# Kernel tuning notes

Hardware: AMD Instinct MI355X
Metric: run time of the kernel (lower is better)

Reference implementation:

```python
import jax, jax.numpy as jnp
import numpy as np

C, H, K, G = 256, 8, 32, 8
HD = C // H
SCALE = HD ** -0.5
POS_BND = int(0.8 * K * 1 ** 0.5)  # 25
RPE_NUM = 2 * POS_BND + 1          # 51
NW = 4096


def setup_inputs() -> dict:
    key = jax.random.key(0)
    ks = jax.random.split(key, 8)
    data = jax.random.normal(ks[0], (NW * (K + G), C), dtype=jnp.float32)
    # relative xyz offsets between points in a window; exercise the clamp
    rel_pos = jax.random.randint(ks[1], (NW, K, K, 3), -POS_BND - 5, POS_BND + 6).astype(jnp.int32)
    # additive mask: 0 for valid pairs, -100 for masked (padded) pairs
    keep = jax.random.bernoulli(ks[2], 0.9, (NW, K + G, K + G))
    mask = jnp.where(keep, 0.0, -100.0).astype(jnp.float32)
    qkv_w = jax.random.normal(ks[3], (C, 3 * C), dtype=jnp.float32) * (C ** -0.5)
    qkv_b = jnp.zeros((3 * C,), dtype=jnp.float32)
    proj_w = jax.random.normal(ks[4], (C, C), dtype=jnp.float32) * (C ** -0.5)
    proj_b = jnp.zeros((C,), dtype=jnp.float32)
    rpe_table = jax.random.normal(ks[5], (3 * RPE_NUM, H), dtype=jnp.float32) * 0.02
    return {"data": data, "rel_pos": rel_pos, "mask": mask, "qkv_w": qkv_w,
            "qkv_b": qkv_b, "proj_w": proj_w, "proj_b": proj_b, "rpe_table": rpe_table}


def reference(data, rel_pos, mask, qkv_w, qkv_b, proj_w, proj_b, rpe_table):
    W = K + G  # window size including context tokens
    qkv = data @ qkv_w + qkv_b                              # (T, 3C)
    qkv_std = jnp.std(qkv, axis=0, ddof=1)                  # torch .std is unbiased
    qkv = qkv.reshape(-1, W, 3, H, HD).transpose(2, 0, 3, 1, 4)  # (3, Nw, H, W, HD)
    q, k, v = qkv[0] * SCALE, qkv[1], qkv[2]
    attn = jnp.einsum('nhqd,nhkd->nhqk', q, k)              # (Nw, H, W, W)
    # RPE: clamp offsets, index per-axis slices of table, sum over xyz
    idx = jnp.clip(rel_pos, -POS_BND, POS_BND) + POS_BND + jnp.arange(3, dtype=rel_pos.dtype) * RPE_NUM
    rpe = rpe_table[idx].sum(axis=3)                        # (Nw, K, K, H)
    rpe = rpe.transpose(0, 3, 1, 2)                         # (Nw, H, K, K)
    rpe = jnp.pad(rpe, ((0, 0), (0, 0), (G, 0), (G, 0)))    # pad for context tokens
    attn = attn + rpe + mask[:, None]
    attn = jax.nn.softmax(attn, axis=-1)
    out = jnp.einsum('nhqk,nhkd->nqhd', attn, v).reshape(-1, W, C)
    out = out @ proj_w + proj_b                             # (Nw, W, C)
    return (out, qkv_std)
```

## Files before the change

### kernel.cpp

```cpp
#include <hip/hip_runtime.h>
#include <math.h>

#define SCALE_F 0.17677669529663687f

typedef __bf16 bf16x8 __attribute__((ext_vector_type(8)));
typedef float f32x4 __attribute__((ext_vector_type(4)));

__device__ __forceinline__ unsigned short f2bf(float f) {
  unsigned u = __builtin_bit_cast(unsigned, f);
  u = (u + 0x7FFFu + ((u >> 16) & 1u)) >> 16;
  return (unsigned short)u;
}
__device__ __forceinline__ float bf2f(unsigned short u) {
  return __builtin_bit_cast(float, (unsigned)u << 16);
}
__device__ __forceinline__ unsigned pk2(float a, float b) {
  return (unsigned)f2bf(a) | ((unsigned)f2bf(b) << 16);
}
__device__ __forceinline__ bf16x8 ld16(const void* p) {
  int4 v = *(const int4*)p;
  return __builtin_bit_cast(bf16x8, v);
}
__device__ __forceinline__ void gll16(const void* g, void* l) {
  __builtin_amdgcn_global_load_lds(
      (const __attribute__((address_space(1))) unsigned int*)g,
      (__attribute__((address_space(3))) unsigned int*)l, 16, 0, 0);
}


__global__ void octa_prep2(const float* __restrict__ qkv_w, const float* __restrict__ proj_w,
                           unsigned short* __restrict__ wTq, unsigned short* __restrict__ pTq)
{
  int e = blockIdx.x * 256 + threadIdx.x;
  if (e < 196608) {
    int nh = e / 98304, rr = e % 98304;
    int kc = rr / 12288, p2 = rr % 12288;
    int n = p2 >> 5, cw = p2 & 31;
    int kl = cw ^ (((n >> 1) & 3) << 3);
    wTq[e] = f2bf(qkv_w[(size_t)(kc * 32 + kl) * 768 + nh * 384 + n]);
  } else {
    int e2 = e - 196608;
    int kc = e2 >> 13, p2 = e2 & 8191;
    int n = p2 >> 5, cw = p2 & 31;
    int kl = cw ^ (((n >> 1) & 3) << 3);
    pTq[e2] = f2bf(proj_w[(size_t)(kc * 32 + kl) * 256 + n]);
  }
}

#define KQ_A  0
#define KQ_B0 32768
#define KQ_B1 57344
#define KQ_E  32768
#define KQ_LDS 81920

__global__ __launch_bounds__(512, 4)
void octa_qkv(const float* __restrict__ data, const float* __restrict__ qkv_b,
              const unsigned short* __restrict__ wTq, float* __restrict__ ws,
              char* __restrict__ qg, char* __restrict__ kg, char* __restrict__ vg)
{
  extern __shared__ char smem[];
  const int tid = threadIdx.x, lane = tid & 63, wid = tid >> 6;
  const int ql = lane & 15, lg = lane >> 4;
  const int bm = blockIdx.x >> 1, nh = blockIdx.x & 1;
  const int wr = wid >> 2, wc = wid & 3;
  const char* wbase = (const char*)wTq + (size_t)nh * 196608;

  #pragma unroll
  for (int it = 0; it < 3; ++it)
    gll16(wbase + wid * 3072 + it * 1024 + lane * 16,
          smem + KQ_B0 + wid * 3072 + it * 1024);
  {
    const float4* src = (const float4*)(data + (size_t)bm * 64 * 256);
    #pragma unroll
    for (int rep = 0; rep < 8; ++rep) {
      int f = rep * 512 + tid;
      int row = f >> 6, q4 = f & 63;
      float4 d4 = src[f];
      *(uint2*)(smem + KQ_A + row * 512 + ((q4 * 8) ^ ((row & 7) << 4))) =
          make_uint2(pk2(d4.x, d4.y), pk2(d4.z, d4.w));
    }
  }
  __syncthreads();

  f32x4 acc[2][6];
  #pragma unroll
  for (int m = 0; m < 2; ++m)
    #pragma unroll
    for (int n = 0; n < 6; ++n) acc[m][n] = (f32x4){0.f, 0.f, 0.f, 0.f};

  #pragma unroll
  for (int t = 0; t < 8; ++t) {
    if (t < 7) {
      char* bb1 = smem + (((t + 1) & 1) ? KQ_B1 : KQ_B0);
      #pragma unroll
      for (int it = 0; it < 3; ++it)
        gll16(wbase + (size_t)(t + 1) * 24576 + wid * 3072 + it * 1024 + lane * 16,
              bb1 + wid * 3072 + it * 1024);
    }
    const char* bb = smem + ((t & 1) ? KQ_B1 : KQ_B0);
    bf16x8 af[2];
    #pragma unroll
    for (int mt = 0; mt < 2; ++mt) {
      int row = wr * 32 + mt * 16 + ql;
      af[mt] = ld16(smem + KQ_A + row * 512 + ((t * 64 + lg * 16) ^ ((row & 7) << 4)));
    }
    #pragma unroll
    for (int nt = 0; nt < 6; ++nt) {
      int n = wc * 96 + nt * 16 + ql;
      bf16x8 bf = ld16(bb + n * 64 + ((lg * 16) ^ (((n >> 1) & 3) << 4)));
      acc[0][nt] = __builtin_amdgcn_mfma_f32_16x16x32_bf16(af[0], bf, acc[0][nt], 0, 0, 0);
      acc[1][nt] = __builtin_amdgcn_mfma_f32_16x16x32_bf16(af[1], bf, acc[1][nt], 0, 0, 0);
    }
    __syncthreads();
  }

  #pragma unroll
  for (int nt = 0; nt < 6; ++nt) {
    int col_l = wc * 96 + nt * 16 + ql;
    int gcol = nh * 384 + col_l;
    int tensor = gcol >> 8;
    float bias = qkv_b[gcol];
    float s1 = 0.f, s2 = 0.f;
    #pragma unroll
    for (int mt = 0; mt < 2; ++mt)
      #pragma unroll
      for (int r = 0; r < 4; ++r) {
        int tok = wr * 32 + mt * 16 + lg * 4 + r;
        float v = acc[mt][nt][r] + bias;
        s1 += v; s2 += v * v;
        float sv = (tensor == 0) ? v * SCALE_F : v;
        *(unsigned short*)(smem + KQ_E + tok * 768 + ((col_l * 2) ^ ((tok & 7) << 4))) = f2bf(sv);
      }
    s1 += __shfl_xor(s1, 16); s1 += __shfl_xor(s1, 32);
    s2 += __shfl_xor(s2, 16); s2 += __shfl_xor(s2, 32);
    if (lg == 0) { atomicAdd(ws + gcol, s1); atomicAdd(ws + 768 + gcol, s2); }
  }
  __syncthreads();

  #pragma unroll
  for (int rep = 0; rep < 6; ++rep) {
    int c = rep * 512 + tid;
    int tok_l = c / 48, cc = c - tok_l * 48;
    int4 val = *(const int4*)(smem + KQ_E + tok_l * 768 + ((cc * 16) ^ ((tok_l & 7) << 4)));
    int gcol0 = nh * 384 + cc * 8;
    int tensor = gcol0 >> 8, h = (gcol0 >> 5) & 7, d0 = gcol0 & 31;
    int tg = bm * 64 + tok_l, w = tg / 40, tk = tg - w * 40;
    size_t slice = (size_t)(w * 8 + h) * 2560;
    char* base = tensor == 0 ? qg : (tensor == 1 ? kg : vg);
    *(int4*)(base + slice + tk * 64 + d0 * 2) = val;
  }
}

#define A2_MSK 0
#define A2_IDX 4160
#define A2_RPT 8256
#define A2_P   13376
#define A2_LDS 44096

__global__ __launch_bounds__(512, 4)
void octa_attn(const char* __restrict__ qg, const char* __restrict__ kg,
               const char* __restrict__ vg, const float* __restrict__ maskp,
               const int* __restrict__ rel_pos, const float* __restrict__ rpe_table,
               char* __restrict__ Og)
{
  extern __shared__ char smem[];
  const int tid = threadIdx.x, w = blockIdx.x, wid = tid >> 6;
  const int lane = tid & 63, ql = lane & 15, lg = lane >> 4, h = wid;
  const int perm = ql * 64 + lg * 16;
  const char* qb = qg + (size_t)(w * 8 + h) * 2560;
  const char* kb = kg + (size_t)(w * 8 + h) * 2560;
  const char* vb = vg + (size_t)(w * 8 + h) * 2560;

  bf16x8 kf0 = ld16(kb + perm), kf1 = ld16(kb + 1024 + perm), kf2 = ld16(kb + 2048 + perm);
  bf16x8 qf0 = ld16(qb + perm), qf1 = ld16(qb + 1024 + perm), qf2 = ld16(qb + 2048 + perm);
  union U8 { unsigned short u[8]; bf16x8 v; };
  U8 ua, ub, uc, ud;
  #pragma unroll
  for (int j = 0; j < 8; ++j) {
    int tok = lg * 8 + j;
    ua.u[j] = *(const unsigned short*)(vb + tok * 64 + ql * 2);
    ub.u[j] = *(const unsigned short*)(vb + tok * 64 + (16 + ql) * 2);
  }
  if (lg == 0) {
    #pragma unroll
    for (int j = 0; j < 8; ++j) {
      uc.u[j] = *(const unsigned short*)(vb + (32 + j) * 64 + ql * 2);
      ud.u[j] = *(const unsigned short*)(vb + (32 + j) * 64 + (16 + ql) * 2);
    }
  } else {
    #pragma unroll
    for (int j = 0; j < 8; ++j) { uc.u[j] = 0; ud.u[j] = 0; }
  }
  bf16x8 vA = ua.v, vB = ub.v, vC = uc.v, vD = ud.v;

  for (int f = tid; f < 1600; f += 512) {
    float m = maskp[(size_t)w * 1600 + f];
    int qi = f / 40, kj = f - qi * 40;
    *(unsigned short*)(smem + A2_MSK + kj * 104 + qi * 2) = f2bf(m);
  }
  for (int f = tid; f < 1024; f += 512) {
    const int* rp = rel_pos + ((size_t)w * 1024 + f) * 3;
    int c0 = rp[0], c1 = rp[1], c2 = rp[2];
    c0 = min(25, max(-25, c0)); c1 = min(25, max(-25, c1)); c2 = min(25, max(-25, c2));
    unsigned pk = (unsigned)(c0 + 25) | ((unsigned)(c1 + 76) << 10) | ((unsigned)(c2 + 127) << 20);
    int qi8 = f >> 5, kj8 = f & 31;
    *(unsigned*)(smem + A2_IDX + kj8 * 128 + ((qi8 * 4) ^ ((kj8 & 1) << 6))) = pk;
  }
  for (int f = tid; f < 1224; f += 512)
    *(float*)(smem + A2_RPT + (((f & 7) * 160 + (f >> 3)) << 2)) = rpe_table[f];
  __syncthreads();

  f32x4 st[9];
  {
    bf16x8 kf[3] = {kf0, kf1, kf2}, qf[3] = {qf0, qf1, qf2};
    #pragma unroll
    for (int a = 0; a < 3; ++a)
      #pragma unroll
      for (int b = 0; b < 3; ++b)
        st[a * 3 + b] = __builtin_amdgcn_mfma_f32_16x16x32_bf16(
            kf[a], qf[b], (f32x4){0.f, 0.f, 0.f, 0.f}, 0, 0, 0);
  }

  float mx[3] = {-3e38f, -3e38f, -3e38f};
  #pragma unroll
  for (int a = 0; a < 3; ++a) {
    #pragma unroll
    for (int b = 0; b < 3; ++b) {
      #pragma unroll
      for (int r = 0; r < 4; ++r) {
        int kj = a * 16 + lg * 4 + r;
        int qi = b * 16 + ql;
        float s = st[a * 3 + b][r];
        if (kj < 40) {
          if (qi < 40) {
            s += bf2f(*(const unsigned short*)(smem + A2_MSK + kj * 104 + qi * 2));
            if (kj >= 8 && qi >= 8) {
              unsigned pk = *(const unsigned*)(smem + A2_IDX + (kj - 8) * 128 +
                                               (((qi - 8) * 4) ^ (((kj - 8) & 1) << 6)));
              s += *(const float*)(smem + A2_RPT + ((h * 160 + (pk & 1023)) << 2))
                 + *(const float*)(smem + A2_RPT + ((h * 160 + ((pk >> 10) & 1023)) << 2))
                 + *(const float*)(smem + A2_RPT + ((h * 160 + (pk >> 20)) << 2));
            }
          }
        } else {
          s = -1e30f;
        }
        st[a * 3 + b][r] = s;
        mx[b] = fmaxf(mx[b], s);
      }
    }
  }
  #pragma unroll
  for (int b = 0; b < 3; ++b) {
    mx[b] = fmaxf(mx[b], __shfl_xor(mx[b], 16));
    mx[b] = fmaxf(mx[b], __shfl_xor(mx[b], 32));
  }
  float sum[3] = {0.f, 0.f, 0.f};
  #pragma unroll
  for (int a = 0; a < 3; ++a)
    #pragma unroll
    for (int b = 0; b < 3; ++b)
      #pragma unroll
      for (int r = 0; r < 4; ++r) {
        float e = __expf(st[a * 3 + b][r] - mx[b]);
        st[a * 3 + b][r] = e;
        sum[b] += e;
      }
  float inv[3];
  #pragma unroll
  for (int b = 0; b < 3; ++b) {
    sum[b] += __shfl_xor(sum[b], 16);
    sum[b] += __shfl_xor(sum[b], 32);
    inv[b] = 1.f / sum[b];
  }

  char* pb_ = smem + A2_P + wid * 3840;
  f32x4 ot[6];
  #pragma unroll
  for (int i = 0; i < 6; ++i) ot[i] = (f32x4){0.f, 0.f, 0.f, 0.f};

  #pragma unroll
  for (int a = 0; a < 2; ++a)
    #pragma unroll
    for (int b = 0; b < 3; ++b)
      #pragma unroll
      for (int r = 0; r < 4; ++r) {
        int kj = a * 16 + lg * 4 + r, qi = b * 16 + ql;
        *(unsigned short*)(pb_ + qi * 80 + kj * 2) = f2bf(st[a * 3 + b][r] * inv[b]);
      }
  asm volatile("" ::: "memory");
  #pragma unroll
  for (int b = 0; b < 3; ++b) {
    bf16x8 pf = ld16(pb_ + (b * 16 + ql) * 80 + lg * 16);
    ot[b]     = __builtin_amdgcn_mfma_f32_16x16x32_bf16(vA, pf, ot[b], 0, 0, 0);
    ot[3 + b] = __builtin_amdgcn_mfma_f32_16x16x32_bf16(vB, pf, ot[3 + b], 0, 0, 0);
  }
  asm volatile("" ::: "memory");
  #pragma unroll
  for (int b = 0; b < 3; ++b) {
    int qi = b * 16 + ql;
    #pragma unroll
    for (int r = 0; r < 4; ++r)
      *(unsigned short*)(pb_ + qi * 80 + (lg * 4 + r) * 2) = f2bf(st[6 + b][r] * inv[b]);
    *(uint2*)(pb_ + qi * 80 + 32 + lg * 8) = make_uint2(0u, 0u);
  }
  asm volatile("" ::: "memory");
  #pragma unroll
  for (int b = 0; b < 3; ++b) {
    bf16x8 pf = ld16(pb_ + (b * 16 + ql) * 80 + lg * 16);
    ot[b]     = __builtin_amdgcn_mfma_f32_16x16x32_bf16(vC, pf, ot[b], 0, 0, 0);
    ot[3 + b] = __builtin_amdgcn_mfma_f32_16x16x32_bf16(vD, pf, ot[3 + b], 0, 0, 0);
  }

  __syncthreads();
  #pragma unroll
  for (int dm = 0; dm < 2; ++dm)
    #pragma unroll
    for (int b = 0; b < 3; ++b) {
      int qi = b * 16 + ql;
      if (b == 2 && ql >= 8) continue;
      unsigned u0 = pk2(ot[dm * 3 + b][0], ot[dm * 3 + b][1]);
      unsigned u1 = pk2(ot[dm * 3 + b][2], ot[dm * 3 + b][3]);
      int tg = w * 40 + qi;
      int colb = (h * 32 + dm * 16 + lg * 4) * 2;
      *(uint2*)(Og + (size_t)tg * 512 + (colb ^ (((tg >> 1) & 3) << 4))) = make_uint2(u0, u1);
    }
}

#define P3_A0 0
#define P3_A1 8192
#define P3_B0 16384
#define P3_B1 32768
#define P3_LDS 49152

__global__ __launch_bounds__(512, 4)
void octa_proj(const char* __restrict__ Og, const unsigned short* __restrict__ pTq,
               const float* __restrict__ proj_b, float* __restrict__ out)
{
  extern __shared__ char smem[];
  const int tid = threadIdx.x, lane = tid & 63, wid = tid >> 6;
  const int ql = lane & 15, lg = lane >> 4;
  const int bm = blockIdx.x;
  const int wr = wid >> 2, wc = wid & 3;
  const char* pbase = (const char*)pTq;

  gll16(Og + ((size_t)bm * 128 + (tid >> 2)) * 512 + (tid & 3) * 16,
        smem + P3_A0 + wid * 1024);
  #pragma unroll
  for (int it = 0; it < 2; ++it)
    gll16(pbase + (wid * 128 + it * 64 + lane) * 16, smem + P3_B0 + wid * 2048 + it * 1024);
  __syncthreads();

  f32x4 acc[4][4];
  #pragma unroll
  for (int m = 0; m < 4; ++m)
    #pragma unroll
    for (int n = 0; n < 4; ++n) acc[m][n] = (f32x4){0.f, 0.f, 0.f, 0.f};

  #pragma unroll
  for (int t = 0; t < 8; ++t) {
    if (t < 7) {
      char* ab1 = smem + (((t + 1) & 1) ? P3_A1 : P3_A0);
      char* bb1 = smem + (((t + 1) & 1) ? P3_B1 : P3_B0);
      gll16(Og + ((size_t)bm * 128 + (tid >> 2)) * 512 + (t + 1) * 64 + (tid & 3) * 16,
            ab1 + wid * 1024);
      #pragma unroll
      for (int it = 0; it < 2; ++it)
        gll16(pbase + (size_t)(t + 1) * 16384 + (wid * 128 + it * 64 + lane) * 16,
              bb1 + wid * 2048 + it * 1024);
    }
    const char* ab = smem + ((t & 1) ? P3_A1 : P3_A0);
    const char* bb = smem + ((t & 1) ? P3_B1 : P3_B0);
    bf16x8 af[4];
    #pragma unroll
    for (int mt = 0; mt < 4; ++mt) {
      int row = wr * 64 + mt * 16 + ql;
      af[mt] = ld16(ab + row * 64 + ((lg * 16) ^ (((row >> 1) & 3) << 4)));
    }
    #pragma unroll
    for (int nt = 0; nt < 4; ++nt) {
      int n = wc * 64 + nt * 16 + ql;
      bf16x8 bf = ld16(bb + n * 64 + ((lg * 16) ^ (((n >> 1) & 3) << 4)));
      #pragma unroll
      for (int mt = 0; mt < 4; ++mt)
        acc[mt][nt] = __builtin_amdgcn_mfma_f32_16x16x32_bf16(af[mt], bf, acc[mt][nt], 0, 0, 0);
    }
    __syncthreads();
  }

  #pragma unroll
  for (int nt = 0; nt < 4; ++nt) {
    int col = wc * 64 + nt * 16 + ql;
    float pb = proj_b[col];
    #pragma unroll
    for (int mt = 0; mt < 4; ++mt)
      #pragma unroll
      for (int r = 0; r < 4; ++r) {
        int tg = bm * 128 + wr * 64 + mt * 16 + lg * 4 + r;
        out[(size_t)tg * 256 + col] = acc[mt][nt][r] + pb;
      }
  }
}

__global__ void octa_std(const float* __restrict__ ws, float* __restrict__ out,
                         int total_rows, size_t off)
{
  int j = blockIdx.x * 256 + threadIdx.x;
  if (j < 768) {
    float s = ws[j], ss = ws[768 + j];
    float T = (float)total_rows;
    float var = (ss - s * s / T) / (T - 1.f);
    out[off + j] = sqrtf(fmaxf(var, 0.f));
  }
}

#define O_RPE 0
#define O_MSK 4896
#define O_IDX 8096
#define O_A   12192
#define O_ATT 36768
#define B1_SZ 49152
#define ATT_STRIDE 11776
#define AK 3840
#define AV 7680
#define B2_S (O_ATT + 94208)
#define B2_A O_ATT
#define LDS_BYTES_V4 163744

__device__ __forceinline__ int a_addr(int row, int byte) {
  return O_A + row * 512 + (byte ^ ((row & 7) << 4));
}
__device__ __forceinline__ int v_addr(int d, int byte) {
  return AV + d * 128 + (byte ^ ((d & 7) << 4));
}

__global__ void octa_prep_v4(const float* __restrict__ qkv_w, const float* __restrict__ proj_w,
                             unsigned short* __restrict__ wTq, unsigned short* __restrict__ pTq)
{
  int idx = blockIdx.x * 256 + threadIdx.x;
  if (idx < 196608) {
    int n = idx >> 8, k = idx & 255;
    wTq[idx] = f2bf(qkv_w[k * 768 + n]);
  } else {
    int i = idx - 196608;
    int n = i >> 8, k = i & 255;
    pTq[i] = f2bf(proj_w[k * 256 + n]);
  }
}

__global__ __launch_bounds__(512, 2)
void octa_main_v4(const float* __restrict__ data, const int* __restrict__ rel_pos,
                  const float* __restrict__ maskp, const float* __restrict__ qkv_b,
                  const float* __restrict__ proj_b, const float* __restrict__ rpe_table,
                  const unsigned short* __restrict__ wTq, const unsigned short* __restrict__ pTq,
                  float* __restrict__ ws, float* __restrict__ out)
{
  extern __shared__ char smem[];
  float* s_rpe = (float*)(smem + O_RPE);
  const int tid = threadIdx.x;
  const int w   = blockIdx.x;
  const int wid = tid >> 6;
  const int lane = tid & 63;
  const int ql = lane & 15;
  const int lg = lane >> 4;
  const int h  = wid;
  const int ab = O_ATT + wid * ATT_STRIDE;

  {
    #pragma unroll
    for (int it = 0; it < 6; ++it) {
      int g = it * 512 + tid;
      int n = g >> 2, slot = g & 3;
      const char* src = (const char*)wTq + (size_t)n * 512 + ((slot * 16) ^ ((n & 3) << 4));
      gll16(src, smem + O_ATT + it * 8192 + wid * 1024);
    }
  }
  for (int f = tid; f < 1224; f += 512) s_rpe[f] = rpe_table[f];
  for (int f = tid; f < 400; f += 512) {
    float4 m4 = ((const float4*)(maskp + (size_t)w * 1600))[f];
    uint2 pk;
    pk.x = pk2(m4.x, m4.y); pk.y = pk2(m4.z, m4.w);
    *(uint2*)(smem + O_MSK + f * 8) = pk;
  }
  for (int p = tid; p < 1024; p += 512) {
    const int* rp = rel_pos + ((size_t)w * 1024 + p) * 3;
    int c0 = rp[0], c1 = rp[1], c2 = rp[2];
    c0 = min(25, max(-25, c0)); c1 = min(25, max(-25, c1)); c2 = min(25, max(-25, c2));
    unsigned pk = (unsigned)(c0 + 25) | ((unsigned)(c1 + 76) << 10) | ((unsigned)(c2 + 127) << 20);
    *(unsigned*)(smem + O_IDX + ((p * 4) ^ (((p >> 5) & 7) << 4))) = pk;
  }
  {
    const float4* src = (const float4*)(data + (size_t)w * 10240);
    for (int f = tid; f < 2560; f += 512) {
      int token = f >> 6, q4 = f & 63;
      float4 d4 = src[f];
      uint2 pk;
      pk.x = pk2(d4.x, d4.y); pk.y = pk2(d4.z, d4.w);
      *(uint2*)(smem + a_addr(token, q4 * 8)) = pk;
    }
    int token = 40 + (tid >> 6), byte = (tid & 63) * 8;
    *(uint2*)(smem + a_addr(token, byte)) = make_uint2(0u, 0u);
  }
  __syncthreads();

  f32x4 acc[18];
  #pragma unroll
  for (int i = 0; i < 18; ++i) acc[i] = (f32x4){0.f, 0.f, 0.f, 0.f};

  for (int t = 0; t < 8; ++t) {
    if (t < 7) {
      int bb = O_ATT + ((t + 1) & 1) * B1_SZ;
      #pragma unroll
      for (int it = 0; it < 6; ++it) {
        int g = it * 512 + tid;
        int n = g >> 2, slot = g & 3;
        const char* src = (const char*)wTq + (size_t)n * 512 + (t + 1) * 64
                          + ((slot * 16) ^ ((n & 3) << 4));
        gll16(src, smem + bb + it * 8192 + wid * 1024);
      }
    }
    const int bb = O_ATT + (t & 1) * B1_SZ;
    bf16x8 af[3];
    #pragma unroll
    for (int mt = 0; mt < 3; ++mt)
      af[mt] = ld16(smem + a_addr(mt * 16 + ql, t * 64 + lg * 16));
    #pragma unroll
    for (int j = 0; j < 6; ++j) {
      int n = ((j >> 1) * 16 + 2 * wid + (j & 1)) * 16 + ql;
      bf16x8 bf = ld16(smem + bb + n * 64 + ((lg * 16) ^ ((n & 3) << 4)));
      #pragma unroll
      for (int mt = 0; mt < 3; ++mt)
        acc[j * 3 + mt] = __builtin_amdgcn_mfma_f32_16x16x32_bf16(af[mt], bf, acc[j * 3 + mt], 0, 0, 0);
    }
    __syncthreads();
  }

  {
    #pragma unroll
    for (int it = 0; it < 4; ++it) {
      int g = it * 512 + tid;
      int n = g >> 3, slot = g & 7;
      const char* src = (const char*)pTq + (size_t)n * 512 + ((slot * 16) ^ ((n & 7) << 4));
      gll16(src, smem + B2_S + it * 8192 + wid * 1024);
    }
  }

  #pragma unroll
  for (int j = 0; j < 6; ++j) {
    int sec = j >> 1;
    int ncol = sec * 256 + 32 * wid + (j & 1) * 16 + ql;
    int d = (j & 1) * 16 + ql;
    float bias = qkv_b[ncol];
    float s1 = 0.f, s2 = 0.f;
    #pragma unroll
    for (int mt = 0; mt < 3; ++mt) {
      #pragma unroll
      for (int r = 0; r < 4; ++r) {
        int token = mt * 16 + lg * 4 + r;
        float v = acc[j * 3 + mt][r] + bias;
        if (token < 40) { s1 += v; s2 += v * v; }
        if (sec == 0)
          *(unsigned short*)(smem + ab + token * 80 + d * 2) = f2bf(v * SCALE_F);
        else if (sec == 1)
          *(unsigned short*)(smem + ab + AK + token * 80 + d * 2) = f2bf(v);
        else
          *(unsigned short*)(smem + ab + v_addr(d, token * 2)) = f2bf(v);
      }
    }
    s1 += __shfl_xor(s1, 16); s1 += __shfl_xor(s1, 32);
    s2 += __shfl_xor(s2, 16); s2 += __shfl_xor(s2, 32);
    if (lg == 0) { atomicAdd(ws + ncol, s1); atomicAdd(ws + 768 + ncol, s2); }
  }
  {
    int zd = lane >> 1;
    int zb = 96 + (lane & 1) * 16;
    *(int4*)(smem + ab + v_addr(zd, zb)) = (int4){0, 0, 0, 0};
  }
  asm volatile("" ::: "memory");

  f32x4 st[9];
  {
    bf16x8 kf[3], qf[3];
    #pragma unroll
    for (int a = 0; a < 3; ++a) kf[a] = ld16(smem + ab + AK + (a * 16 + ql) * 80 + lg * 16);
    #pragma unroll
    for (int b = 0; b < 3; ++b) qf[b] = ld16(smem + ab + (b * 16 + ql) * 80 + lg * 16);
    #pragma unroll
    for (int a = 0; a < 3; ++a)
      #pragma unroll
      for (int b = 0; b < 3; ++b)
        st[a * 3 + b] = __builtin_amdgcn_mfma_f32_16x16x32_bf16(
            kf[a], qf[b], (f32x4){0.f, 0.f, 0.f, 0.f}, 0, 0, 0);
  }

  float mx[3] = {-3e38f, -3e38f, -3e38f};
  #pragma unroll
  for (int a = 0; a < 3; ++a) {
    #pragma unroll
    for (int b = 0; b < 3; ++b) {
      #pragma unroll
      for (int r = 0; r < 4; ++r) {
        int kj = a * 16 + lg * 4 + r;
        int qi = b * 16 + ql;
        float s = st[a * 3 + b][r];
        if (kj < 40) {
          if (qi < 40) {
            s += bf2f(*(const unsigned short*)(smem + O_MSK + (qi * 40 + kj) * 2));
            if (kj >= 8 && qi >= 8) {
              int p = (qi - 8) * 32 + (kj - 8);
              unsigned pk = *(const unsigned*)(smem + O_IDX + ((p * 4) ^ (((p >> 5) & 7) << 4)));
              s += s_rpe[(pk & 1023) * 8 + h] + s_rpe[((pk >> 10) & 1023) * 8 + h]
                 + s_rpe[(pk >> 20) * 8 + h];
            }
          }
        } else {
          s = -1e30f;
        }
        st[a * 3 + b][r] = s;
        mx[b] = fmaxf(mx[b], s);
      }
    }
  }
  #pragma unroll
  for (int b = 0; b < 3; ++b) {
    mx[b] = fmaxf(mx[b], __shfl_xor(mx[b], 16));
    mx[b] = fmaxf(mx[b], __shfl_xor(mx[b], 32));
  }
  float sum[3] = {0.f, 0.f, 0.f};
  #pragma unroll
  for (int a = 0; a < 3; ++a)
    #pragma unroll
    for (int b = 0; b < 3; ++b)
      #pragma unroll
      for (int r = 0; r < 4; ++r) {
        float e = __expf(st[a * 3 + b][r] - mx[b]);
        st[a * 3 + b][r] = e;
        sum[b] += e;
      }
  float inv[3];
  #pragma unroll
  for (int b = 0; b < 3; ++b) {
    sum[b] += __shfl_xor(sum[b], 16);
    sum[b] += __shfl_xor(sum[b], 32);
    inv[b] = 1.f / sum[b];
  }

  f32x4 ot[6];
  #pragma unroll
  for (int i = 0; i < 6; ++i) ot[i] = (f32x4){0.f, 0.f, 0.f, 0.f};

  #pragma unroll
  for (int a = 0; a < 2; ++a)
    #pragma unroll
    for (int b = 0; b < 3; ++b)
      #pragma unroll
      for (int r = 0; r < 4; ++r) {
        int kj = a * 16 + lg * 4 + r, qi = b * 16 + ql;
        *(unsigned short*)(smem + ab + qi * 80 + kj * 2) = f2bf(st[a * 3 + b][r] * inv[b]);
      }
  asm volatile("" ::: "memory");
  {
    bf16x8 vf0 = ld16(smem + ab + v_addr(ql, lg * 16));
    bf16x8 vf1 = ld16(smem + ab + v_addr(16 + ql, lg * 16));
    #pragma unroll
    for (int b = 0; b < 3; ++b) {
      bf16x8 pf = ld16(smem + ab + (b * 16 + ql) * 80 + lg * 16);
      ot[b] = __builtin_amdgcn_mfma_f32_16x16x32_bf16(vf0, pf, ot[b], 0, 0, 0);
      ot[3 + b] = __builtin_amdgcn_mfma_f32_16x16x32_bf16(vf1, pf, ot[3 + b], 0, 0, 0);
    }
  }
  asm volatile("" ::: "memory");
  #pragma unroll
  for (int b = 0; b < 3; ++b) {
    int qi = b * 16 + ql;
    #pragma unroll
    for (int r = 0; r < 4; ++r) {
      int kj = 32 + lg * 4 + r;
      *(unsigned short*)(smem + ab + qi * 80 + (kj - 32) * 2) = f2bf(st[6 + b][r] * inv[b]);
    }
    *(uint2*)(smem + ab + qi * 80 + 32 + lg * 8) = make_uint2(0u, 0u);
  }
  asm volatile("" ::: "memory");
  {
    bf16x8 vf0 = ld16(smem + ab + v_addr(ql, 64 + lg * 16));
    bf16x8 vf1 = ld16(smem + ab + v_addr(16 + ql, 64 + lg * 16));
    #pragma unroll
    for (int b = 0; b < 3; ++b) {
      bf16x8 pf = ld16(smem + ab + (b * 16 + ql) * 80 + lg * 16);
      ot[b] = __builtin_amdgcn_mfma_f32_16x16x32_bf16(vf0, pf, ot[b], 0, 0, 0);
      ot[3 + b] = __builtin_amdgcn_mfma_f32_16x16x32_bf16(vf1, pf, ot[3 + b], 0, 0, 0);
    }
  }
  #pragma unroll
  for (int dm = 0; dm < 2; ++dm)
    #pragma unroll
    for (int b = 0; b < 3; ++b)
      #pragma unroll
      for (int r = 0; r < 4; ++r) {
        int d = dm * 16 + lg * 4 + r;
        int qi = b * 16 + ql;
        *(unsigned short*)(smem + a_addr(qi, (h * 32 + d) * 2)) = f2bf(ot[dm * 3 + b][r]);
      }
  __syncthreads();

  f32x4 oacc[6];
  #pragma unroll
  for (int i = 0; i < 6; ++i) oacc[i] = (f32x4){0.f, 0.f, 0.f, 0.f};

  for (int t = 0; t < 4; ++t) {
    if (t < 3) {
      int bb = ((t + 1) & 1) ? B2_A : B2_S;
      #pragma unroll
      for (int it = 0; it < 4; ++it) {
        int g = it * 512 + tid;
        int n = g >> 3, slot = g & 7;
        const char* src = (const char*)pTq + (size_t)n * 512 + (t + 1) * 128
                          + ((slot * 16) ^ ((n & 7) << 4));
        gll16(src, smem + bb + it * 8192 + wid * 1024);
      }
    }
    const int bb = (t & 1) ? B2_A : B2_S;
    #pragma unroll
    for (int ks = 0; ks < 2; ++ks) {
      bf16x8 af[3];
      #pragma unroll
      for (int mt = 0; mt < 3; ++mt)
        af[mt] = ld16(smem + a_addr(mt * 16 + ql, t * 128 + ks * 64 + lg * 16));
      #pragma unroll
      for (int nt = 0; nt < 2; ++nt) {
        int n = (2 * wid + nt) * 16 + ql;
        bf16x8 bf = ld16(smem + bb + n * 128 + ((ks * 64 + lg * 16) ^ ((n & 7) << 4)));
        #pragma unroll
        for (int mt = 0; mt < 3; ++mt)
          oacc[nt * 3 + mt] = __builtin_amdgcn_mfma_f32_16x16x32_bf16(af[mt], bf, oacc[nt * 3 + mt], 0, 0, 0);
      }
    }
    __syncthreads();
  }

  #pragma unroll
  for (int nt = 0; nt < 2; ++nt) {
    int ncol = (2 * wid + nt) * 16 + ql;
    float pb = proj_b[ncol];
    #pragma unroll
    for (int mt = 0; mt < 3; ++mt)
      #pragma unroll
      for (int r = 0; r < 4; ++r) {
        int token = mt * 16 + lg * 4 + r;
        if (token < 40)
          out[(size_t)w * 10240 + token * 256 + ncol] = oacc[nt * 3 + mt][r] + pb;
      }
  }
}

extern "C" void kernel_launch(void* const* d_in, const int* in_sizes, int n_in,
                              void* d_out, int out_size, void* d_ws, size_t ws_size,
                              hipStream_t stream) {
  const float* data    = (const float*)d_in[0];
  const int*   rel_pos = (const int*)d_in[1];
  const float* maskp   = (const float*)d_in[2];
  const float* qkv_w   = (const float*)d_in[3];
  const float* qkv_b   = (const float*)d_in[4];
  const float* proj_w  = (const float*)d_in[5];
  const float* proj_b  = (const float*)d_in[6];
  const float* rpe_tab = (const float*)d_in[7];
  float* out = (float*)d_out;
  float* ws  = (float*)d_ws;

  const int nw = in_sizes[1] / 3072;
  const int total_rows = nw * 40;
  const size_t std_off = (size_t)nw * 10240;

  const size_t WS_NEED = 530432ull + 83886080ull;

  unsigned short* wTq = (unsigned short*)((char*)d_ws + 6144);
  unsigned short* pTq = (unsigned short*)((char*)d_ws + 399360);

  hipMemsetAsync(ws, 0, 6144, stream);

  if (ws_size >= WS_NEED) {
    char* kg = (char*)d_ws + 530432;
    char* Og = kg;
    char* qg = (char*)d_out;
    char* vg = (char*)d_out + 83886080;

    (void)hipFuncSetAttribute((const void*)octa_qkv,
                              hipFuncAttributeMaxDynamicSharedMemorySize, KQ_LDS);

    hipLaunchKernelGGL(octa_prep2, dim3(1024), dim3(256), 0, stream, qkv_w, proj_w, wTq, pTq);
    hipLaunchKernelGGL(octa_qkv, dim3(nw * 40 / 64 * 2), dim3(512), KQ_LDS, stream,
                       data, qkv_b, wTq, ws, qg, kg, vg);
    hipLaunchKernelGGL(octa_attn, dim3(nw), dim3(512), A2_LDS, stream,
                       qg, kg, vg, maskp, rel_pos, rpe_tab, Og);
    hipLaunchKernelGGL(octa_proj, dim3(nw * 40 / 128), dim3(512), P3_LDS, stream,
                       Og, pTq, proj_b, out);
    hipLaunchKernelGGL(octa_std, dim3(3), dim3(256), 0, stream, ws, out, total_rows, std_off);
  } else {
    hipLaunchKernelGGL(octa_prep_v4, dim3(1024), dim3(256), 0, stream, qkv_w, proj_w, wTq, pTq);
    (void)hipFuncSetAttribute((const void*)octa_main_v4,
                              hipFuncAttributeMaxDynamicSharedMemorySize, LDS_BYTES_V4);
    hipLaunchKernelGGL(octa_main_v4, dim3(nw), dim3(512), LDS_BYTES_V4, stream,
                       data, rel_pos, maskp, qkv_b, proj_b, rpe_tab, wTq, pTq, ws, out);
    hipLaunchKernelGGL(octa_std, dim3(3), dim3(256), 0, stream, ws, out, total_rows, std_off);
  }
}
```

Baseline: 399.1 us.

## Retile QKV GEMM to 128x256 blocks with pipelined A tiles and direct stores

The QKV projection kernel moves from 64-row by 384-column tiles to 128-row by 256-column tiles, so each block produces exactly one of Q, K or V. The activation tile is now double-buffered per K-chunk, with the next chunk loaded into registers during the MFMAs, instead of staging the whole 64x256 block up front. LDS use drops from 80KB to 48KB, which may allow more resident blocks. The epilogue writes scattered 2-byte values straight to global memory instead of staging through LDS for 16-byte stores, which risks poorer write coalescing.

```diff
diff --git a/kernel.cpp b/kernel.cpp
--- a/kernel.cpp
+++ b/kernel.cpp
@@ -33,11 +33,12 @@
 {
   int e = blockIdx.x * 256 + threadIdx.x;
   if (e < 196608) {
-    int nh = e / 98304, rr = e % 98304;
-    int kc = rr / 12288, p2 = rr % 12288;
+    int c = e >> 13;
+    int nc = c >> 3, kc = c & 7;
+    int p2 = e & 8191;
     int n = p2 >> 5, cw = p2 & 31;
     int kl = cw ^ (((n >> 1) & 3) << 3);
-    wTq[e] = f2bf(qkv_w[(size_t)(kc * 32 + kl) * 768 + nh * 384 + n]);
+    wTq[e] = f2bf(qkv_w[(size_t)(kc * 32 + kl) * 768 + nc * 256 + n]);
   } else {
     int e2 = e - 196608;
     int kc = e2 >> 13, p2 = e2 & 8191;
@@ -47,11 +48,11 @@
   }
 }
 
-#define KQ_A  0
-#define KQ_B0 32768
-#define KQ_B1 57344
-#define KQ_E  32768
-#define KQ_LDS 81920
+#define KQ_A0 0
+#define KQ_A1 8192
+#define KQ_B0 16384
+#define KQ_B1 32768
+#define KQ_LDS 49152
 
 __global__ __launch_bounds__(512, 4)
 void octa_qkv(const float* __restrict__ data, const float* __restrict__ qkv_b,
@@ -61,93 +62,91 @@
   extern __shared__ char smem[];
   const int tid = threadIdx.x, lane = tid & 63, wid = tid >> 6;
   const int ql = lane & 15, lg = lane >> 4;
-  const int bm = blockIdx.x >> 1, nh = blockIdx.x & 1;
+  const int bm = blockIdx.x / 3, nc = blockIdx.x - bm * 3;
   const int wr = wid >> 2, wc = wid & 3;
-  const char* wbase = (const char*)wTq + (size_t)nh * 196608;
-
-  #pragma unroll
-  for (int it = 0; it < 3; ++it)
-    gll16(wbase + wid * 3072 + it * 1024 + lane * 16,
-          smem + KQ_B0 + wid * 3072 + it * 1024);
-  {
-    const float4* src = (const float4*)(data + (size_t)bm * 64 * 256);
-    #pragma unroll
-    for (int rep = 0; rep < 8; ++rep) {
-      int f = rep * 512 + tid;
-      int row = f >> 6, q4 = f & 63;
-      float4 d4 = src[f];
-      *(uint2*)(smem + KQ_A + row * 512 + ((q4 * 8) ^ ((row & 7) << 4))) =
-          make_uint2(pk2(d4.x, d4.y), pk2(d4.z, d4.w));
-    }
-  }
+  const char* wbase = (const char*)wTq + (size_t)nc * 131072;
+
+  const int arow = tid >> 2, aq = tid & 3;
+  const float* abase = data + ((size_t)bm * 128 + arow) * 256 + aq * 8;
+  const int alds = arow * 64 + ((aq * 16) ^ (((arow >> 1) & 3) << 4));
+
+  float4 a0 = *(const float4*)abase;
+  float4 a1 = *(const float4*)(abase + 4);
+  gll16(wbase + wid * 1024 + lane * 16, smem + KQ_B0 + wid * 1024);
+  gll16(wbase + 8192 + wid * 1024 + lane * 16, smem + KQ_B0 + 8192 + wid * 1024);
+  *(uint2*)(smem + KQ_A0 + alds) = make_uint2(pk2(a0.x, a0.y), pk2(a0.z, a0.w));
+  *(uint2*)(smem + KQ_A0 + alds + 8) = make_uint2(pk2(a1.x, a1.y), pk2(a1.z, a1.w));
   __syncthreads();
 
-  f32x4 acc[2][6];
-  #pragma unroll
-  for (int m = 0; m < 2; ++m)
-    #pragma unroll
-    for (int n = 0; n < 6; ++n) acc[m][n] = (f32x4){0.f, 0.f, 0.f, 0.f};
+  f32x4 acc[4][4];
+  #pragma unroll
+  for (int m = 0; m < 4; ++m)
+    #pragma unroll
+    for (int n = 0; n < 4; ++n) acc[m][n] = (f32x4){0.f, 0.f, 0.f, 0.f};
 
   #pragma unroll
   for (int t = 0; t < 8; ++t) {
+    float4 na0, na1;
     if (t < 7) {
+      na0 = *(const float4*)(abase + (t + 1) * 32);
+      na1 = *(const float4*)(abase + (t + 1) * 32 + 4);
+      const char* bsrc = wbase + (size_t)(t + 1) * 16384;
       char* bb1 = smem + (((t + 1) & 1) ? KQ_B1 : KQ_B0);
-      #pragma unroll
-      for (int it = 0; it < 3; ++it)
-        gll16(wbase + (size_t)(t + 1) * 24576 + wid * 3072 + it * 1024 + lane * 16,
-              bb1 + wid * 3072 + it * 1024);
-    }
+      gll16(bsrc + wid * 1024 + lane * 16, bb1 + wid * 1024);
+      gll16(bsrc + 8192 + wid * 1024 + lane * 16, bb1 + 8192 + wid * 1024);
+    }
+    const char* ab = smem + ((t & 1) ? KQ_A1 : KQ_A0);
     const char* bb = smem + ((t & 1) ? KQ_B1 : KQ_B0);
-    bf16x8 af[2];
-    #pragma unroll
-    for (int mt = 0; mt < 2; ++mt) {
-      int row = wr * 32 + mt * 16 + ql;
-      af[mt] = ld16(smem + KQ_A + row * 512 + ((t * 64 + lg * 16) ^ ((row & 7) << 4)));
-    }
-    #pragma unroll
-    for (int nt = 0; nt < 6; ++nt) {
-      int n = wc * 96 + nt * 16 + ql;
-      bf16x8 bf = ld16(bb + n * 64 + ((lg * 16) ^ (((n >> 1) & 3) << 4)));
-      acc[0][nt] = __builtin_amdgcn_mfma_f32_16x16x32_bf16(af[0], bf, acc[0][nt], 0, 0, 0);
-      acc[1][nt] = __builtin_amdgcn_mfma_f32_16x16x32_bf16(af[1], bf, acc[1][nt], 0, 0, 0);
+    bf16x8 af[4], bf[4];
+    #pragma unroll
+    for (int mt = 0; mt < 4; ++mt) {
+      int row = wr * 64 + mt * 16 + ql;
+      af[mt] = ld16(ab + row * 64 + ((lg * 16) ^ (((row >> 1) & 3) << 4)));
+    }
+    #pragma unroll
+    for (int nt = 0; nt < 4; ++nt) {
+      int n = wc * 64 + nt * 16 + ql;
+      bf[nt] = ld16(bb + n * 64 + ((lg * 16) ^ (((n >> 1) & 3) << 4)));
+    }
+    #pragma unroll
+    for (int nt = 0; nt < 4; ++nt)
+      #pragma unroll
+      for (int mt = 0; mt < 4; ++mt)
+        acc[mt][nt] = __builtin_amdgcn_mfma_f32_16x16x32_bf16(af[mt], bf[nt], acc[mt][nt], 0, 0, 0);
+    if (t < 7) {
+      char* ab1 = smem + (((t + 1) & 1) ? KQ_A1 : KQ_A0);
+      *(uint2*)(ab1 + alds) = make_uint2(pk2(na0.x, na0.y), pk2(na0.z, na0.w));
+      *(uint2*)(ab1 + alds + 8) = make_uint2(pk2(na1.x, na1.y), pk2(na1.z, na1.w));
     }
     __syncthreads();
   }
 
-  #pragma unroll
-  for (int nt = 0; nt < 6; ++nt) {
-    int col_l = wc * 96 + nt * 16 + ql;
-    int gcol = nh * 384 + col_l;
-    int tensor = gcol >> 8;
-    float bias = qkv_b[gcol];
+  char* base = nc == 0 ? qg : (nc == 1 ? kg : vg);
+  const float cs = (nc == 0) ? SCALE_F : 1.0f;
+  #pragma unroll
+  for (int nt = 0; nt < 4; ++nt) {
+    int col = wc * 64 + nt * 16 + ql;
+    int h = col >> 5, d = col & 31;
+    float bias = qkv_b[nc * 256 + col];
     float s1 = 0.f, s2 = 0.f;
     #pragma unroll
-    for (int mt = 0; mt < 2; ++mt)
-      #pragma unroll
-      for (int r = 0; r < 4; ++r) {
-        int tok = wr * 32 + mt * 16 + lg * 4 + r;
+    for (int mt = 0; mt < 4; ++mt) {
+      int tg0 = bm * 128 + wr * 64 + mt * 16 + lg * 4;
+      int w = tg0 / 40, tk0 = tg0 - w * 40;
+      size_t slice = (size_t)(w * 8 + h) * 2560;
+      #pragma unroll
+      for (int r = 0; r < 4; ++r) {
         float v = acc[mt][nt][r] + bias;
         s1 += v; s2 += v * v;
-        float sv = (tensor == 0) ? v * SCALE_F : v;
-        *(unsigned short*)(smem + KQ_E + tok * 768 + ((col_l * 2) ^ ((tok & 7) << 4))) = f2bf(sv);
-      }
+        *(unsigned short*)(base + slice + (tk0 + r) * 64 + d * 2) = f2bf(v * cs);
+      }
+    }
     s1 += __shfl_xor(s1, 16); s1 += __shfl_xor(s1, 32);
     s2 += __shfl_xor(s2, 16); s2 += __shfl_xor(s2, 32);
-    if (lg == 0) { atomicAdd(ws + gcol, s1); atomicAdd(ws + 768 + gcol, s2); }
-  }
-  __syncthreads();
-
-  #pragma unroll
-  for (int rep = 0; rep < 6; ++rep) {
-    int c = rep * 512 + tid;
-    int tok_l = c / 48, cc = c - tok_l * 48;
-    int4 val = *(const int4*)(smem + KQ_E + tok_l * 768 + ((cc * 16) ^ ((tok_l & 7) << 4)));
-    int gcol0 = nh * 384 + cc * 8;
-    int tensor = gcol0 >> 8, h = (gcol0 >> 5) & 7, d0 = gcol0 & 31;
-    int tg = bm * 64 + tok_l, w = tg / 40, tk = tg - w * 40;
-    size_t slice = (size_t)(w * 8 + h) * 2560;
-    char* base = tensor == 0 ? qg : (tensor == 1 ? kg : vg);
-    *(int4*)(base + slice + tk * 64 + d0 * 2) = val;
+    if (lg == 0) {
+      atomicAdd(ws + nc * 256 + col, s1);
+      atomicAdd(ws + 768 + nc * 256 + col, s2);
+    }
   }
 }
 
@@ -784,11 +783,8 @@
     char* qg = (char*)d_out;
     char* vg = (char*)d_out + 83886080;
 
-    (void)hipFuncSetAttribute((const void*)octa_qkv,
-                              hipFuncAttributeMaxDynamicSharedMemorySize, KQ_LDS);
-
     hipLaunchKernelGGL(octa_prep2, dim3(1024), dim3(256), 0, stream, qkv_w, proj_w, wTq, pTq);
-    hipLaunchKernelGGL(octa_qkv, dim3(nw * 40 / 64 * 2), dim3(512), KQ_LDS, stream,
+    hipLaunchKernelGGL(octa_qkv, dim3(nw * 40 / 128 * 3), dim3(512), KQ_LDS, stream,
                        data, qkv_b, wTq, ws, qg, kg, vg);
     hipLaunchKernelGGL(octa_attn, dim3(nw), dim3(512), A2_LDS, stream,
                        qg, kg, vg, maskp, rel_pos, rpe_tab, Og);
```

Result: faster. 381.2 us (-4.5%).
